# Performance work log

Measured on AMD Instinct MI355X. Metric: run time of the kernel, lower is better.

## Reference

```python
import jax, jax.numpy as jnp
import numpy as np

SIGMA = 3.0          # vdW clash radius
HB_R0 = 2.9          # ideal N..O hbond distance
HB_SIG2 = 0.2 ** 2   # hbond gaussian width^2
EPS = 1e-6


def setup_inputs() -> dict:
    key = jax.random.key(0)
    k1, k2 = jax.random.split(key)
    coords = jax.random.normal(k1, (8, 512, 4, 3), dtype=jnp.float32)
    motors = jax.random.normal(k2, (8, 512, 8), dtype=jnp.float32)
    mask = jnp.ones((8, 512), dtype=jnp.float32)
    return {"coords": coords, "motors": motors, "mask": mask}


def _energy(coords, motors, mask):
    B, S, A, _ = coords.shape
    dt = coords.dtype

    # ---- vdW repulsion over all atom pairs: [B, S*A, S*A] ----
    flat = coords.reshape(B, S * A, 3)
    fmask = jnp.repeat(mask, A, axis=1)                       # [B, S*A]
    dist_sq = jnp.sum((flat[:, :, None, :] - flat[:, None, :, :]) ** 2, axis=-1)
    r = jnp.sqrt(dist_sq + EPS)
    overlap = jnp.maximum(SIGMA - r, 0.0)
    clash = overlap ** 4
    pair_mask = fmask[:, :, None] * fmask[:, None, :]
    pair_mask = pair_mask * (1.0 - jnp.eye(S * A, dtype=dt)[None])
    lj = jnp.sum(clash * pair_mask) / (jnp.sum(pair_mask) + EPS)

    # ---- hydrogen-bond energy: N (atom 0) vs O (atom 3), [B, S, S] ----
    Nc = coords[:, :, 0, :]
    Oc = coords[:, :, 3, :]
    dist = jnp.sqrt(jnp.sum((Nc[:, :, None, :] - Oc[:, None, :, :]) ** 2, axis=-1))
    h_energy = jnp.exp(-0.5 * (dist - HB_R0) ** 2 / HB_SIG2)
    idx = jnp.arange(S)
    range_mask = (jnp.abs(idx[None, :] - idx[:, None]) > 2).astype(dt)
    pm = mask[:, :, None] * mask[:, None, :] * range_mask[None]
    hb = -jnp.sum(h_energy * pm) / (jnp.sum(mask) + EPS)

    # ---- motor smoothness ----
    diff = jnp.sum((motors[:, 1:] - motors[:, :-1]) ** 2, axis=-1)
    m_mask = mask[:, 1:] * mask[:, :-1]
    motor = jnp.sum(diff * m_mask) / (jnp.sum(m_mask) + EPS)

    # ---- radius of gyration on CA (atom 1) ----
    ca = coords[:, :, 1, :]
    msum = jnp.sum(mask, axis=1, keepdims=True)               # [B,1]
    mean_pos = jnp.sum(ca * mask[:, :, None], axis=1) / (msum + EPS)
    d2 = jnp.sum((ca - mean_pos[:, None, :]) ** 2, axis=-1)
    rg_sq = jnp.sum(d2 * mask, axis=1) / (msum[:, 0] + EPS)
    rg = jnp.mean(rg_sq)

    return 1.0 * lj + 0.5 * hb + 0.1 * motor + 0.05 * rg


def reference(coords, motors, mask):
    return _energy(coords, motors, mask)
```

## Files before the change

### kernel.cpp

```cpp
#include <hip/hip_runtime.h>
#include <hip/hip_bf16.h>
#include <math.h>

#define B 8
#define S 512
#define A 4
#define N (S*A)
#define SIGMA 3.0f
#define HB_R0 2.9f
#define HB_COEF (-12.5f)
#define EPS 1e-6f

#define NLJ 576
#define NHB 64
#define NAUX 8
#define NPART (NLJ + NHB + NAUX)

#define WS_LJ   0
#define WS_HB   1
#define WS_CNT  4
#define WS_AUX  8
#define POISON_U 0xAAAAAAAAu

__device__ __forceinline__ float wave_reduce_sum(float v) {
    #pragma unroll
    for (int off = 32; off > 0; off >>= 1) v += __shfl_down(v, off, 64);
    return v;
}

__device__ __forceinline__ void acc_add(float* p, float v) {
    __hip_atomic_fetch_add(p, v, __ATOMIC_RELAXED, __HIP_MEMORY_SCOPE_AGENT);
}
__device__ __forceinline__ void slot_store(float* p, float v) {
    __hip_atomic_store(p, v, __ATOMIC_RELAXED, __HIP_MEMORY_SCOPE_AGENT);
}
__device__ __forceinline__ float slot_load(const float* p) {
    return __hip_atomic_load(p, __ATOMIC_RELAXED, __HIP_MEMORY_SCOPE_AGENT);
}

__global__ __launch_bounds__(256) void physics_fused(
        const float* __restrict__ coords,
        const float* __restrict__ motors,
        const float* __restrict__ mask,
        float* __restrict__ ws,
        float* __restrict__ out) {
    const int bid = blockIdx.x;
    const int tid = threadIdx.x;

    __shared__ float4 sj[128];
    __shared__ float  redbuf[32];

    const int wid = tid >> 6, lane = tid & 63;
    unsigned int* counter = (unsigned int*)(ws + WS_CNT);

    if (bid < NLJ) {
        const int b    = bid / 72;
        const int r    = bid % 72;
        const int p    = r >> 1;
        const int half = r & 1;
        int it = 0, pp = p;
        while (pp >= 8 - it) { pp -= 8 - it; ++it; }
        const int jt = it + pp;

        const float* cb = coords + (size_t)b * N * 3;
        const float* mb = mask + b * S;
        const int jlo = jt * 256 + half * 128;

        if (tid < 128) {
            const int j = jlo + tid;
            sj[tid] = make_float4(cb[j*3+0], cb[j*3+1], cb[j*3+2], mb[j >> 2]);
        }
        __syncthreads();

        const int i = it * 256 + tid;
        const float xi = cb[i*3+0], yi = cb[i*3+1], zi = cb[i*3+2];
        const float fmi = mb[i >> 2];

        float acc = 0.f;
        #pragma unroll 8
        for (int jj = 0; jj < 128; ++jj) {
            const float4 q = sj[jj];
            const float dx = xi - q.x;
            const float dy = yi - q.y;
            const float dz = zi - q.z;
            const float d2 = fmaf(dx, dx, fmaf(dy, dy, fmaf(dz, dz, EPS)));
            const float rr = __builtin_amdgcn_sqrtf(d2);
            const float ov = fmaxf(SIGMA - rr, 0.f);
            const float ov2 = ov * ov;
            acc = fmaf(ov2 * ov2, q.w, acc);
        }
        if (it == jt && i >= jlo && i < jlo + 128) {
            const float ovd = SIGMA - __builtin_amdgcn_sqrtf(EPS);
            const float o2 = ovd * ovd;
            acc -= fmi * (o2 * o2);
        }
        float v = fmi * acc;
        if (it != jt) v *= 2.f;

        v = wave_reduce_sum(v);
        if (lane == 0) redbuf[wid] = v;
        __syncthreads();
        if (tid == 0)
            acc_add(ws + WS_LJ, redbuf[0] + redbuf[1] + redbuf[2] + redbuf[3]);

    } else if (bid < NLJ + NHB) {
        const int idx = bid - NLJ;
        const int b  = idx >> 3;
        const int rr_ = idx & 7;
        const int it = rr_ >> 2;
        const int jh = rr_ & 3;

        const float* cb = coords + (size_t)b * S * A * 3;
        const float* mb = mask + b * S;
        const int jlo = jh * 128;

        if (tid < 128) {
            const int j = jlo + tid;
            sj[tid] = make_float4(cb[(j*4+3)*3+0], cb[(j*4+3)*3+1],
                                  cb[(j*4+3)*3+2], mb[j]);
        }
        __syncthreads();

        const int i = it * 256 + tid;
        const float xi = cb[(i*4+0)*3+0];
        const float yi = cb[(i*4+0)*3+1];
        const float zi = cb[(i*4+0)*3+2];
        const float mi = mb[i];

        float acc = 0.f;
        #pragma unroll 8
        for (int jj = 0; jj < 128; ++jj) {
            const float4 q = sj[jj];
            const float dx = xi - q.x;
            const float dy = yi - q.y;
            const float dz = zi - q.z;
            const float d2 = fmaf(dx, dx, fmaf(dy, dy, dz * dz));
            const float dist = __builtin_amdgcn_sqrtf(d2);
            const float t = dist - HB_R0;
            const float e = __expf(HB_COEF * (t * t));
            acc = fmaf(e, q.w, acc);
        }
        #pragma unroll
        for (int dj = -2; dj <= 2; ++dj) {
            const int j = i + dj;
            if (j >= jlo && j < jlo + 128) {
                const float4 q = sj[j - jlo];
                const float dx = xi - q.x;
                const float dy = yi - q.y;
                const float dz = zi - q.z;
                const float d2 = fmaf(dx, dx, fmaf(dy, dy, dz * dz));
                const float dist = __builtin_amdgcn_sqrtf(d2);
                const float t = dist - HB_R0;
                const float e = __expf(HB_COEF * (t * t));
                acc -= e * q.w;
            }
        }
        float v = mi * acc;
        v = wave_reduce_sum(v);
        if (lane == 0) redbuf[wid] = v;
        __syncthreads();
        if (tid == 0)
            acc_add(ws + WS_HB, redbuf[0] + redbuf[1] + redbuf[2] + redbuf[3]);

    } else {
        const int b = bid - NLJ - NHB;
        const float* cb = coords + (size_t)b * S * A * 3;
        const float* mb = mask + b * S;

        float s1x = 0.f, s1y = 0.f, s1z = 0.f, s2 = 0.f, M = 0.f, Sm2 = 0.f;
        float mn = 0.f, md = 0.f;

        for (int s = tid; s < S; s += 256) {
            const float m = mb[s];
            const float* ca = cb + ((size_t)(s*4 + 1)) * 3;
            const float x = ca[0], y = ca[1], z = ca[2];
            s1x = fmaf(x, m, s1x);
            s1y = fmaf(y, m, s1y);
            s1z = fmaf(z, m, s1z);
            s2  = fmaf(fmaf(x, x, fmaf(y, y, z * z)), m, s2);
            M   += m;
            Sm2 = fmaf(m, m, Sm2);
            if (s < S - 1) {
                const float mm = m * mb[s + 1];
                const float4* m4 = (const float4*)(motors + ((size_t)b * S + s) * 8);
                const float4 a0 = m4[0], a1 = m4[1], b0 = m4[2], b1 = m4[3];
                float d = 0.f;
                float df;
                df = b0.x - a0.x; d = fmaf(df, df, d);
                df = b0.y - a0.y; d = fmaf(df, df, d);
                df = b0.z - a0.z; d = fmaf(df, df, d);
                df = b0.w - a0.w; d = fmaf(df, df, d);
                df = b1.x - a1.x; d = fmaf(df, df, d);
                df = b1.y - a1.y; d = fmaf(df, df, d);
                df = b1.z - a1.z; d = fmaf(df, df, d);
                df = b1.w - a1.w; d = fmaf(df, df, d);
                mn = fmaf(d, mm, mn);
                md += mm;
            }
        }

        float vals[8] = {s1x, s1y, s1z, s2, M, Sm2, mn, md};
        #pragma unroll
        for (int k = 0; k < 8; ++k) {
            float v = wave_reduce_sum(vals[k]);
            if (lane == 0) redbuf[wid * 8 + k] = v;
        }
        __syncthreads();
        if (tid < 8) {
            const float t = redbuf[tid] + redbuf[8 + tid] + redbuf[16 + tid] + redbuf[24 + tid];
            slot_store(ws + WS_AUX + b * 8 + tid, t);
        }
    }

    if (tid == 0) {
        const unsigned int ret = __hip_atomic_fetch_add(
            counter, 1u, __ATOMIC_RELEASE, __HIP_MEMORY_SCOPE_AGENT);
        const bool last = (ret == POISON_U + (NPART - 1u)) ||
                          (ret == (unsigned int)(NPART - 1));
        if (last) {
            __threadfence();

            const float lj_num = slot_load(ws + WS_LJ);
            const float hb_num = slot_load(ws + WS_HB);

            float lj_den = 0.f, masksum = 0.f, mnum = 0.f, mden = 0.f, rg = 0.f;
            #pragma unroll
            for (int b = 0; b < B; ++b) {
                float p[8];
                #pragma unroll
                for (int k = 0; k < 8; ++k)
                    p[k] = slot_load(ws + WS_AUX + b * 8 + k);
                const float M = p[4], Sm2 = p[5];
                lj_den  += 16.f * M * M - 4.f * Sm2;
                masksum += M;
                mnum    += p[6];
                mden    += p[7];
                const float Me = M + EPS;
                const float mx = p[0] / Me, my = p[1] / Me, mz = p[2] / Me;
                const float d2sum = p[3] - 2.f * (mx * p[0] + my * p[1] + mz * p[2])
                                  + (mx * mx + my * my + mz * mz) * M;
                rg += d2sum / Me;
            }
            rg *= (1.f / (float)B);

            const float ljv   = lj_num / (lj_den + EPS);
            const float hbv   = -hb_num / (masksum + EPS);
            const float motor = mnum / (mden + EPS);
            out[0] = ljv + 0.5f * hbv + 0.1f * motor + 0.05f * rg;
        }
    }
}

extern "C" void kernel_launch(void* const* d_in, const int* in_sizes, int n_in,
                              void* d_out, int out_size, void* d_ws, size_t ws_size,
                              hipStream_t stream) {
    const float* coords = (const float*)d_in[0];
    const float* motors = (const float*)d_in[1];
    const float* mask   = (const float*)d_in[2];
    float* ws  = (float*)d_ws;
    float* out = (float*)d_out;

    physics_fused<<<NPART, 256, 0, stream>>>(coords, motors, mask, ws, out);
}
```

Measured before the change: 79.35 us.

## Compute full LJ pair matrix in 256 blocks and deterministic slot-based reduction

Replaces the triangular 576-block LJ decomposition plus separate HB/aux blocks with 256 uniform blocks, each covering 256 i atoms against 512 j atoms. HB and aux work is piggybacked onto the first 72 of those blocks. Float atomics are replaced by per-block partial slots, and the last block reduces them in parallel. This does double the LJ arithmetic (no symmetry reuse) in exchange for fewer blocks, no atomic contention and a single wave of work. Blocks 0-71 now carry extra HB/aux work, which may create stragglers.

```diff
diff --git a/kernel.cpp b/kernel.cpp
--- a/kernel.cpp
+++ b/kernel.cpp
@@ -11,15 +11,12 @@
 #define HB_COEF (-12.5f)
 #define EPS 1e-6f
 
-#define NLJ 576
-#define NHB 64
-#define NAUX 8
-#define NPART (NLJ + NHB + NAUX)
+#define NPROD 256
 
 #define WS_LJ   0
-#define WS_HB   1
-#define WS_CNT  4
-#define WS_AUX  8
+#define WS_HB   256
+#define WS_AUX  320
+#define WS_CNT  448
 #define POISON_U 0xAAAAAAAAu
 
 __device__ __forceinline__ float wave_reduce_sum(float v) {
@@ -28,9 +25,6 @@
     return v;
 }
 
-__device__ __forceinline__ void acc_add(float* p, float v) {
-    __hip_atomic_fetch_add(p, v, __ATOMIC_RELAXED, __HIP_MEMORY_SCOPE_AGENT);
-}
 __device__ __forceinline__ void slot_store(float* p, float v) {
     __hip_atomic_store(p, v, __ATOMIC_RELAXED, __HIP_MEMORY_SCOPE_AGENT);
 }
@@ -47,28 +41,28 @@
     const int bid = blockIdx.x;
     const int tid = threadIdx.x;
 
-    __shared__ float4 sj[128];
+    __shared__ float4 sj[512];
     __shared__ float  redbuf[32];
+    __shared__ float  saux[64];
+    __shared__ int    winflag;
 
     const int wid = tid >> 6, lane = tid & 63;
     unsigned int* counter = (unsigned int*)(ws + WS_CNT);
 
-    if (bid < NLJ) {
-        const int b    = bid / 72;
-        const int r    = bid % 72;
-        const int p    = r >> 1;
-        const int half = r & 1;
-        int it = 0, pp = p;
-        while (pp >= 8 - it) { pp -= 8 - it; ++it; }
-        const int jt = it + pp;
+    {
+        const int b  = bid >> 5;
+        const int it = (bid >> 2) & 7;
+        const int jc = bid & 3;
 
         const float* cb = coords + (size_t)b * N * 3;
         const float* mb = mask + b * S;
-        const int jlo = jt * 256 + half * 128;
-
-        if (tid < 128) {
-            const int j = jlo + tid;
-            sj[tid] = make_float4(cb[j*3+0], cb[j*3+1], cb[j*3+2], mb[j >> 2]);
+        const int jlo = jc * 512;
+
+        {
+            const int j0 = jlo + tid;
+            sj[tid]       = make_float4(cb[j0*3+0], cb[j0*3+1], cb[j0*3+2], mb[j0 >> 2]);
+            const int j1 = j0 + 256;
+            sj[tid + 256] = make_float4(cb[j1*3+0], cb[j1*3+1], cb[j1*3+2], mb[j1 >> 2]);
         }
         __syncthreads();
 
@@ -78,7 +72,7 @@
 
         float acc = 0.f;
         #pragma unroll 8
-        for (int jj = 0; jj < 128; ++jj) {
+        for (int jj = 0; jj < 512; ++jj) {
             const float4 q = sj[jj];
             const float dx = xi - q.x;
             const float dy = yi - q.y;
@@ -89,22 +83,21 @@
             const float ov2 = ov * ov;
             acc = fmaf(ov2 * ov2, q.w, acc);
         }
-        if (it == jt && i >= jlo && i < jlo + 128) {
+        if ((it >> 1) == jc) {
             const float ovd = SIGMA - __builtin_amdgcn_sqrtf(EPS);
             const float o2 = ovd * ovd;
             acc -= fmi * (o2 * o2);
         }
-        float v = fmi * acc;
-        if (it != jt) v *= 2.f;
-
-        v = wave_reduce_sum(v);
+        float v = wave_reduce_sum(fmi * acc);
         if (lane == 0) redbuf[wid] = v;
         __syncthreads();
         if (tid == 0)
-            acc_add(ws + WS_LJ, redbuf[0] + redbuf[1] + redbuf[2] + redbuf[3]);
-
-    } else if (bid < NLJ + NHB) {
-        const int idx = bid - NLJ;
+            slot_store(ws + WS_LJ + bid, redbuf[0] + redbuf[1] + redbuf[2] + redbuf[3]);
+        __syncthreads();
+    }
+
+    if (bid < 64) {
+        const int idx = bid;
         const int b  = idx >> 3;
         const int rr_ = idx & 7;
         const int it = rr_ >> 2;
@@ -155,15 +148,14 @@
                 acc -= e * q.w;
             }
         }
-        float v = mi * acc;
-        v = wave_reduce_sum(v);
+        float v = wave_reduce_sum(mi * acc);
         if (lane == 0) redbuf[wid] = v;
         __syncthreads();
         if (tid == 0)
-            acc_add(ws + WS_HB, redbuf[0] + redbuf[1] + redbuf[2] + redbuf[3]);
-
-    } else {
-        const int b = bid - NLJ - NHB;
+            slot_store(ws + WS_HB + idx, redbuf[0] + redbuf[1] + redbuf[2] + redbuf[3]);
+
+    } else if (bid < 72) {
+        const int b = bid - 64;
         const float* cb = coords + (size_t)b * S * A * 3;
         const float* mb = mask + b * S;
 
@@ -212,24 +204,36 @@
         }
     }
 
+    __syncthreads();
     if (tid == 0) {
+        __atomic_signal_fence(__ATOMIC_SEQ_CST);
+        __builtin_amdgcn_s_waitcnt(0);
+        __atomic_signal_fence(__ATOMIC_SEQ_CST);
         const unsigned int ret = __hip_atomic_fetch_add(
-            counter, 1u, __ATOMIC_RELEASE, __HIP_MEMORY_SCOPE_AGENT);
-        const bool last = (ret == POISON_U + (NPART - 1u)) ||
-                          (ret == (unsigned int)(NPART - 1));
-        if (last) {
-            __threadfence();
-
-            const float lj_num = slot_load(ws + WS_LJ);
-            const float hb_num = slot_load(ws + WS_HB);
+            counter, 1u, __ATOMIC_RELAXED, __HIP_MEMORY_SCOPE_AGENT);
+        winflag = (ret == POISON_U + (NPROD - 1u)) ||
+                  (ret == (unsigned int)(NPROD - 1)) ? 1 : 0;
+    }
+    __syncthreads();
+
+    if (winflag) {
+        float lj = slot_load(ws + WS_LJ + tid);
+        float hb = (tid < 64) ? slot_load(ws + WS_HB + tid) : 0.f;
+        if (tid < 64) saux[tid] = slot_load(ws + WS_AUX + tid);
+
+        lj = wave_reduce_sum(lj);
+        hb = wave_reduce_sum(hb);
+        if (lane == 0) { redbuf[wid * 2 + 0] = lj; redbuf[wid * 2 + 1] = hb; }
+        __syncthreads();
+
+        if (tid == 0) {
+            const float lj_num = redbuf[0] + redbuf[2] + redbuf[4] + redbuf[6];
+            const float hb_num = redbuf[1] + redbuf[3] + redbuf[5] + redbuf[7];
 
             float lj_den = 0.f, masksum = 0.f, mnum = 0.f, mden = 0.f, rg = 0.f;
             #pragma unroll
             for (int b = 0; b < B; ++b) {
-                float p[8];
-                #pragma unroll
-                for (int k = 0; k < 8; ++k)
-                    p[k] = slot_load(ws + WS_AUX + b * 8 + k);
+                const float* p = saux + b * 8;
                 const float M = p[4], Sm2 = p[5];
                 lj_den  += 16.f * M * M - 4.f * Sm2;
                 masksum += M;
@@ -260,5 +264,5 @@
     float* ws  = (float*)d_ws;
     float* out = (float*)d_out;
 
-    physics_fused<<<NPART, 256, 0, stream>>>(coords, motors, mask, ws, out);
-}
+    physics_fused<<<NPROD, 256, 0, stream>>>(coords, motors, mask, ws, out);
+}
```

Measured after the change: 82.18 us. 3.6% more time.
